# Kernel optimization log

Hardware: AMD Instinct MI355X
Metric: run time of the kernel (lower is better)

The kernel has to match this reference:

```python
import jax, jax.numpy as jnp
import numpy as np

D_MODEL = 512
EPS = 1e-5  # torch LayerNorm default


def _layernorm(x, g, b):
    mu = jnp.mean(x, axis=-1, keepdims=True)
    var = jnp.mean(jnp.square(x - mu), axis=-1, keepdims=True)
    return (x - mu) * jax.lax.rsqrt(var + EPS) * g + b


def setup_inputs() -> dict:
    key = jax.random.key(0)
    ks = jax.random.split(key, 12)
    d = D_MODEL
    s = 1.0 / np.sqrt(d)
    s4 = 1.0 / np.sqrt(4 * d)
    return {
        "x": jax.random.normal(ks[0], (4, 4096, d), dtype=jnp.float32),
        "Wq": jax.random.uniform(ks[1], (d, d), jnp.float32, -s, s),
        "bq": jax.random.uniform(ks[2], (d,), jnp.float32, -s, s),
        "Wk": jax.random.uniform(ks[3], (d, d), jnp.float32, -s, s),
        "bk": jax.random.uniform(ks[4], (d,), jnp.float32, -s, s),
        "Wv": jax.random.uniform(ks[5], (d, d), jnp.float32, -s, s),
        "bv": jax.random.uniform(ks[6], (d,), jnp.float32, -s, s),
        "g1": jnp.ones((d,), jnp.float32),
        "b1": jnp.zeros((d,), jnp.float32),
        "g2": jnp.ones((d,), jnp.float32),
        "b2": jnp.zeros((d,), jnp.float32),
        "W1": jax.random.uniform(ks[7], (d, 4 * d), jnp.float32, -s, s),
        "bf1": jax.random.uniform(ks[8], (4 * d,), jnp.float32, -s, s),
        "W2": jax.random.uniform(ks[9], (4 * d, d), jnp.float32, -s4, s4),
        "bf2": jax.random.uniform(ks[10], (d,), jnp.float32, -s4, s4),
    }


def reference(x, Wq, bq, Wk, bk, Wv, bv, g1, b1, g2, b2, W1, bf1, W2, bf2):
    # QKV projections: [b, s, d]
    Q = jnp.einsum("bsd,de->bse", x, Wq) + bq
    K = jnp.einsum("bsd,de->bse", x, Wk) + bk
    V = jnp.einsum("bsd,de->bse", x, Wv) + bv
    scale = 1.0 / jnp.sqrt(jnp.float32(K.shape[-1]))
    scores = jnp.einsum("bqd,bkd->bqk", Q, K) * scale  # [b, s, s]
    attn = jax.nn.softmax(scores, axis=-1)
    att = jnp.einsum("bqk,bkd->bqd", attn, V)
    x = _layernorm(x + att, g1, b1)
    h = jax.nn.relu(jnp.einsum("bsd,df->bsf", x, W1) + bf1)
    ffn = jnp.einsum("bsf,fd->bsd", h, W2) + bf2
    return _layernorm(x + ffn, g2, b2)
```

## Files before the change

### kernel.cpp

```cpp
#include <hip/hip_runtime.h>
#include <hip/hip_bf16.h>

typedef unsigned short u16;
typedef short bf16x8 __attribute__((ext_vector_type(8)));
typedef float f32x4 __attribute__((ext_vector_type(4)));

__device__ __forceinline__ float b2f(u16 u) {
  union { float f; unsigned int i; } v; v.i = ((unsigned int)u) << 16; return v.f;
}
__device__ __forceinline__ u16 f2b(float f) {
  union { float f; unsigned int i; } v; v.f = f;
  unsigned int r = v.i + 0x7fffu + ((v.i >> 16) & 1u);
  return (u16)(r >> 16);
}
__device__ __forceinline__ u16 to_b(float v) { return f2b(v); }
__device__ __forceinline__ u16 to_b(u16 v) { return v; }
__device__ __forceinline__ float to_f(float v) { return v; }
__device__ __forceinline__ float to_f(u16 v) { return b2f(v); }

__device__ __forceinline__ void gl_lds16(const u16* g, u16* l) {
  __builtin_amdgcn_global_load_lds(
      (const __attribute__((address_space(1))) unsigned int*)g,
      (__attribute__((address_space(3))) unsigned int*)l, 16, 0, 0);
}

template <bool RELU, bool ATOMIC>
__global__ __launch_bounds__(256)
void gemm_nt(const u16* __restrict__ A, const u16* __restrict__ Bt,
             const float* __restrict__ bias, void* __restrict__ Cv,
             int N, int K, int nsplit, int lda, int ldb, int ldc,
             long sA, long sB, long sC, float scale) {
  __shared__ __align__(16) u16 As[128 * 64];
  __shared__ __align__(16) u16 Bs[128 * 64];
  const int z = blockIdx.z;
  const int batch = z / nsplit, split = z - batch * nsplit;
  const int Ks = K / nsplit;
  const u16* Ab = A + (long)batch * sA + (long)split * Ks;
  const u16* Bb = Bt + (long)batch * sB + (long)split * Ks;
  const int m0 = blockIdx.y * 128, n0 = blockIdx.x * 128;
  const int t = threadIdx.x, w = t >> 6, lane = t & 63;
  const int wm = (w >> 1) * 64, wn = (w & 1) * 64;
  const int lr = lane & 15, q = lane >> 4;

  int srow[4], scol[4];
#pragma unroll
  for (int i = 0; i < 4; i++) {
    int n = w * 256 + i * 64 + lane;
    srow[i] = n >> 3;
    scol[i] = (((n & 7) ^ ((n >> 3) & 7)) * 8);
  }

  f32x4 acc[4][4];
#pragma unroll
  for (int i = 0; i < 4; i++)
#pragma unroll
    for (int j = 0; j < 4; j++) acc[i][j] = (f32x4){0.f, 0.f, 0.f, 0.f};

  for (int k0 = 0; k0 < Ks; k0 += 64) {
#pragma unroll
    for (int i = 0; i < 4; i++)
      gl_lds16(Ab + (long)(m0 + srow[i]) * lda + k0 + scol[i], &As[(w * 256 + i * 64) * 8]);
#pragma unroll
    for (int i = 0; i < 4; i++)
      gl_lds16(Bb + (long)(n0 + srow[i]) * ldb + k0 + scol[i], &Bs[(w * 256 + i * 64) * 8]);
    __syncthreads();
#pragma unroll
    for (int kk = 0; kk < 2; kk++) {
      bf16x8 af[4], bfr[4];
#pragma unroll
      for (int i = 0; i < 4; i++) {
        int row = wm + i * 16 + lr;
        af[i] = *(const bf16x8*)&As[row * 64 + (((kk * 4 + q) ^ (row & 7)) * 8)];
      }
#pragma unroll
      for (int j = 0; j < 4; j++) {
        int row = wn + j * 16 + lr;
        bfr[j] = *(const bf16x8*)&Bs[row * 64 + (((kk * 4 + q) ^ (row & 7)) * 8)];
      }
#pragma unroll
      for (int i = 0; i < 4; i++)
#pragma unroll
        for (int j = 0; j < 4; j++)
          acc[i][j] = __builtin_amdgcn_mfma_f32_16x16x32_bf16(af[i], bfr[j], acc[i][j], 0, 0, 0);
    }
    __syncthreads();
  }

#pragma unroll
  for (int j = 0; j < 4; j++) {
    int cg = n0 + wn + j * 16 + lr;
    float bb = (!ATOMIC && bias) ? bias[cg] : 0.0f;
#pragma unroll
    for (int i = 0; i < 4; i++) {
      int rbase = m0 + wm + i * 16 + q * 4;
#pragma unroll
      for (int r = 0; r < 4; r++) {
        float vv = acc[i][j][r] * scale;
        if (ATOMIC) {
          atomicAdd((float*)Cv + (long)batch * sC + (long)(rbase + r) * ldc + cg, vv);
        } else {
          vv += bb;
          if (RELU) vv = fmaxf(vv, 0.0f);
          ((u16*)Cv)[(long)batch * sC + (long)(rbase + r) * ldc + cg] = f2b(vv);
        }
      }
    }
  }
}

__global__ __launch_bounds__(256, 2)
void flash_attn(const u16* __restrict__ QKV, const u16* __restrict__ Vt,
                u16* __restrict__ attp, float* __restrict__ lbp, float scl) {
  __shared__ __align__(16) u16 buf[128 * 128];
  const int qt = blockIdx.x;
  const int half = blockIdx.y;
  const int batch = blockIdx.z;
  const int t = threadIdx.x, w = t >> 6, lane = t & 63;
  const int lr = lane & 15, q = lane >> 4;
  const long rowbase = (long)batch * 4096 + qt * 64;
  const u16* Qrow  = QKV + (rowbase + w * 16 + lr) * 1536;
  const u16* Kbase = QKV + ((long)batch * 4096 + half * 2048) * 1536 + 512;
  const u16* Vtb   = Vt + (long)batch * 512 * 4096 + half * 2048;
  u16* Pw = buf + w * (16 * 136);

  f32x4 O[32];
#pragma unroll
  for (int i = 0; i < 32; i++) O[i] = (f32x4){0.f, 0.f, 0.f, 0.f};
  float lsum[4] = {0.f, 0.f, 0.f, 0.f};

  for (int kv = 0; kv < 16; kv++) {
    f32x4 S[8];
#pragma unroll
    for (int j = 0; j < 8; j++) S[j] = (f32x4){0.f, 0.f, 0.f, 0.f};

    for (int kc = 0; kc < 4; kc++) {
#pragma unroll
      for (int rr = 0; rr < 8; rr++) {
        int n = rr * 256 + t;
        int row = n >> 4, c = (n & 15) ^ (row & 15);
        gl_lds16(Kbase + (long)(kv * 128 + row) * 1536 + kc * 128 + c * 8,
                 &buf[(rr * 256 + w * 64) * 8]);
      }
      bf16x8 Qf[4];
#pragma unroll
      for (int ss = 0; ss < 4; ss++)
        Qf[ss] = *(const bf16x8*)(Qrow + kc * 128 + ss * 32 + q * 8);
      __syncthreads();
#pragma unroll
      for (int ss = 0; ss < 4; ss++)
#pragma unroll
        for (int j = 0; j < 8; j++) {
          int row = j * 16 + lr;
          bf16x8 Kf = *(const bf16x8*)&buf[row * 128 + (((ss * 4 + q) ^ lr) * 8)];
          S[j] = __builtin_amdgcn_mfma_f32_16x16x32_bf16(Qf[ss], Kf, S[j], 0, 0, 0);
        }
      __syncthreads();
    }

    float psum[4] = {0.f, 0.f, 0.f, 0.f};
#pragma unroll
    for (int j = 0; j < 8; j++)
#pragma unroll
      for (int r = 0; r < 4; r++) {
        float e = __expf(S[j][r] * scl);
        psum[r] += e;
        Pw[(q * 4 + r) * 136 + j * 16 + lr] = f2b(e);
      }
#pragma unroll
    for (int r = 0; r < 4; r++) {
#pragma unroll
      for (int o = 1; o < 16; o <<= 1) psum[r] += __shfl_xor(psum[r], o);
      lsum[r] += psum[r];
    }
    bf16x8 Pf[4];
#pragma unroll
    for (int t4 = 0; t4 < 4; t4++)
      Pf[t4] = *(const bf16x8*)&Pw[lr * 136 + t4 * 32 + q * 8];
    __syncthreads();

    for (int dc = 0; dc < 4; dc++) {
#pragma unroll
      for (int rr = 0; rr < 8; rr++) {
        int n = rr * 256 + t;
        int row = n >> 4, c = (n & 15) ^ (row & 15);
        gl_lds16(Vtb + (long)(dc * 128 + row) * 4096 + kv * 128 + c * 8,
                 &buf[(rr * 256 + w * 64) * 8]);
      }
      __syncthreads();
#pragma unroll
      for (int t4 = 0; t4 < 4; t4++)
#pragma unroll
        for (int j = 0; j < 8; j++) {
          int row = j * 16 + lr;
          bf16x8 Vf = *(const bf16x8*)&buf[row * 128 + (((t4 * 4 + q) ^ lr) * 8)];
          O[dc * 8 + j] = __builtin_amdgcn_mfma_f32_16x16x32_bf16(Pf[t4], Vf, O[dc * 8 + j], 0, 0, 0);
        }
      __syncthreads();
    }
  }

  u16* op = attp + (long)half * 16384 * 512;
#pragma unroll
  for (int i = 0; i < 32; i++) {
    int col = (i >> 3) * 128 + (i & 7) * 16 + lr;
#pragma unroll
    for (int r = 0; r < 4; r++)
      op[(rowbase + w * 16 + q * 4 + r) * 512 + col] = f2b(O[i][r]);
  }
  if (lr == 0)
#pragma unroll
    for (int r = 0; r < 4; r++)
      lbp[(long)half * 16384 + rowbase + w * 16 + q * 4 + r] = lsum[r];
}

template <typename TS>
__global__ __launch_bounds__(1024)
void transpose_b(const TS* __restrict__ src, u16* __restrict__ dst,
                 int R, int Cc, int src_ld, long sbs, long dbs) {
  __shared__ u16 tile[32][33];
  int r = blockIdx.y * 32 + threadIdx.y;
  int c = blockIdx.x * 32 + threadIdx.x;
  tile[threadIdx.y][threadIdx.x] = to_b(src[(long)blockIdx.z * sbs + (long)r * src_ld + c]);
  __syncthreads();
  int rr = blockIdx.x * 32 + threadIdx.y;
  int cc = blockIdx.y * 32 + threadIdx.x;
  dst[(long)blockIdx.z * dbs + (long)rr * R + cc] = tile[threadIdx.x][threadIdx.y];
}

__global__ __launch_bounds__(256)
void f32_to_bf16(const float* __restrict__ s, u16* __restrict__ d) {
  long i = ((long)blockIdx.x * 256 + threadIdx.x) * 8;
  float4 a0 = *(const float4*)(s + i);
  float4 a1 = *(const float4*)(s + i + 4);
  u16 tmp[8] = {f2b(a0.x), f2b(a0.y), f2b(a0.z), f2b(a0.w),
                f2b(a1.x), f2b(a1.y), f2b(a1.z), f2b(a1.w)};
  *(uint4*)(d + i) = *(uint4*)tmp;
}

__global__ __launch_bounds__(256)
void add_ln_att(const float* __restrict__ X, const u16* __restrict__ attp,
                const float* __restrict__ lbp,
                const float* __restrict__ g, const float* __restrict__ b,
                u16* __restrict__ O) {
  const int row = blockIdx.x * 4 + (threadIdx.x >> 6);
  const int lane = threadIdx.x & 63;
  const size_t base = (size_t)row * 512 + lane * 8;
  const float inv = 1.0f / (lbp[row] + lbp[16384 + row]);
  uint4 p0 = *(const uint4*)(attp + base);
  uint4 p1 = *(const uint4*)(attp + 16384L * 512 + base);
  const u16* s0 = (const u16*)&p0;
  const u16* s1 = (const u16*)&p1;
  float z[8];
  float s1a = 0.f, s2a = 0.f;
#pragma unroll
  for (int i = 0; i < 8; i++) {
    z[i] = X[base + i] + (b2f(s0[i]) + b2f(s1[i])) * inv;
    s1a += z[i]; s2a += z[i] * z[i];
  }
#pragma unroll
  for (int o = 32; o > 0; o >>= 1) { s1a += __shfl_xor(s1a, o); s2a += __shfl_xor(s2a, o); }
  const float mu = s1a * (1.0f / 512.0f);
  const float var = s2a * (1.0f / 512.0f) - mu * mu;
  const float rstd = rsqrtf(var + 1e-5f);
#pragma unroll
  for (int i = 0; i < 8; i++) {
    int c = lane * 8 + i;
    O[base + i] = f2b((z[i] - mu) * rstd * g[c] + b[c]);
  }
}

template <typename TX, typename TR, bool EB, typename TO>
__global__ __launch_bounds__(256)
void add_ln(const TX* __restrict__ X, const TR* __restrict__ Rr,
            const float* __restrict__ eb,
            const float* __restrict__ g, const float* __restrict__ b,
            TO* __restrict__ O) {
  const int row = blockIdx.x * 4 + (threadIdx.x >> 6);
  const int lane = threadIdx.x & 63;
  const size_t base = (size_t)row * 512 + lane * 8;
  float z[8];
  float s1 = 0.f, s2 = 0.f;
#pragma unroll
  for (int i = 0; i < 8; i++) {
    int c = lane * 8 + i;
    z[i] = to_f(X[base + i]) + to_f(Rr[base + i]) + (EB ? eb[c] : 0.0f);
    s1 += z[i]; s2 += z[i] * z[i];
  }
#pragma unroll
  for (int o = 32; o > 0; o >>= 1) { s1 += __shfl_xor(s1, o); s2 += __shfl_xor(s2, o); }
  const float mu = s1 * (1.0f / 512.0f);
  const float var = s2 * (1.0f / 512.0f) - mu * mu;
  const float rstd = rsqrtf(var + 1e-5f);
#pragma unroll
  for (int i = 0; i < 8; i++) {
    int c = lane * 8 + i;
    float vv = (z[i] - mu) * rstd * g[c] + b[c];
    if (sizeof(TO) == 2) ((u16*)O)[base + i] = f2b(vv);
    else ((float*)O)[base + i] = vv;
  }
}

__global__ __launch_bounds__(256)
void concat3(const float* __restrict__ a, const float* __restrict__ b,
             const float* __restrict__ c, float* __restrict__ o) {
  int i = threadIdx.x + blockIdx.x * 256;
  if (i < 512) o[i] = a[i];
  else if (i < 1024) o[i] = b[i - 512];
  else if (i < 1536) o[i] = c[i - 1024];
}

extern "C" void kernel_launch(void* const* d_in, const int* in_sizes, int n_in,
                              void* d_out, int out_size, void* d_ws, size_t ws_size,
                              hipStream_t stream) {
  const float* x   = (const float*)d_in[0];
  const float* Wq  = (const float*)d_in[1];
  const float* bq  = (const float*)d_in[2];
  const float* Wk  = (const float*)d_in[3];
  const float* bk  = (const float*)d_in[4];
  const float* Wv  = (const float*)d_in[5];
  const float* bv  = (const float*)d_in[6];
  const float* g1  = (const float*)d_in[7];
  const float* b1  = (const float*)d_in[8];
  const float* g2  = (const float*)d_in[9];
  const float* b2  = (const float*)d_in[10];
  const float* W1  = (const float*)d_in[11];
  const float* bf1 = (const float*)d_in[12];
  const float* W2  = (const float*)d_in[13];
  const float* bf2 = (const float*)d_in[14];
  float* out = (float*)d_out;

  char* ws = (char*)d_ws;
  const size_t MB = 1048576;
  u16*   QKV   = (u16*)(ws + 0);
  u16*   Vt    = (u16*)(ws + 48 * MB);
  u16*   attp  = (u16*)(ws + 64 * MB);
  u16*   h     = (u16*)(ws + 64 * MB);
  float* lbp   = (float*)(ws + 128 * MB);
  u16*   x1    = (u16*)(ws + 129 * MB);
  float* ffnf  = (float*)(ws + 145 * MB);
  u16*   xb    = (u16*)(ws + 145 * MB);
  u16*   wqkvt = (u16*)(ws + 177 * MB);
  u16*   w1t   = wqkvt + 1536 * 512;
  u16*   w2t   = w1t + 2048 * 512;
  float* bqkv  = (float*)(w2t + 512 * 2048);

  dim3 tb(32, 32);
  f32_to_bf16<<<4096, 256, 0, stream>>>(x, xb);
  transpose_b<float><<<dim3(16, 16, 1), tb, 0, stream>>>(Wq, wqkvt,              512, 512, 512, 0, 0);
  transpose_b<float><<<dim3(16, 16, 1), tb, 0, stream>>>(Wk, wqkvt + 512 * 512,  512, 512, 512, 0, 0);
  transpose_b<float><<<dim3(16, 16, 1), tb, 0, stream>>>(Wv, wqkvt + 1024 * 512, 512, 512, 512, 0, 0);
  transpose_b<float><<<dim3(64, 16, 1), tb, 0, stream>>>(W1, w1t, 512, 2048, 2048, 0, 0);
  transpose_b<float><<<dim3(16, 64, 1), tb, 0, stream>>>(W2, w2t, 2048, 512, 512, 0, 0);
  concat3<<<6, 256, 0, stream>>>(bq, bk, bv, bqkv);

  gemm_nt<false, false><<<dim3(12, 128, 1), 256, 0, stream>>>(
      xb, wqkvt, bqkv, QKV, 1536, 512, 1, 512, 512, 1536, 0, 0, 0, 1.0f);

  transpose_b<u16><<<dim3(16, 128, 4), tb, 0, stream>>>(
      QKV + 1024, Vt, 4096, 512, 1536, 4096L * 1536, 512L * 4096);

  const float scl = 0.044194173824159216f;
  flash_attn<<<dim3(64, 2, 4), 256, 0, stream>>>(QKV, Vt, attp, lbp, scl);

  add_ln_att<<<4096, 256, 0, stream>>>(x, attp, lbp, g1, b1, x1);
  gemm_nt<true, false><<<dim3(16, 128, 1), 256, 0, stream>>>(
      x1, w1t, bf1, h, 2048, 512, 1, 512, 512, 2048, 0, 0, 0, 1.0f);
  hipMemsetAsync(ffnf, 0, 32 * MB, stream);
  gemm_nt<false, true><<<dim3(4, 128, 2), 256, 0, stream>>>(
      h, w2t, nullptr, ffnf, 512, 2048, 2, 2048, 2048, 512, 0, 0, 0, 1.0f);
  add_ln<u16, float, true, float><<<4096, 256, 0, stream>>>(
      x1, ffnf, bf2, g2, b2, out);
}
```

Baseline: 610.0 us.

## Split attention KV four ways and replace atomic FFN2 split-K with bf16 partials

The flash attention kernel now splits the key/value range into four quarters instead of two. That doubles the grid, and the launch bound rises to 4 blocks per CU to improve occupancy; the attention add+LayerNorm kernel sums four partial outputs and four row sums. The second FFN GEMM no longer memsets an fp32 buffer and accumulates with atomics. Instead it writes two bf16 split-K partials that a new fused add+LayerNorm kernel combines with the bias. The higher occupancy target may cause register spills in the attention kernel, and the bf16 partials lose some precision.

```diff
diff --git a/kernel.cpp b/kernel.cpp
--- a/kernel.cpp
+++ b/kernel.cpp
@@ -108,19 +108,19 @@
   }
 }
 
-__global__ __launch_bounds__(256, 2)
+__global__ __launch_bounds__(256, 4)
 void flash_attn(const u16* __restrict__ QKV, const u16* __restrict__ Vt,
                 u16* __restrict__ attp, float* __restrict__ lbp, float scl) {
   __shared__ __align__(16) u16 buf[128 * 128];
   const int qt = blockIdx.x;
-  const int half = blockIdx.y;
+  const int quar = blockIdx.y;
   const int batch = blockIdx.z;
   const int t = threadIdx.x, w = t >> 6, lane = t & 63;
   const int lr = lane & 15, q = lane >> 4;
   const long rowbase = (long)batch * 4096 + qt * 64;
   const u16* Qrow  = QKV + (rowbase + w * 16 + lr) * 1536;
-  const u16* Kbase = QKV + ((long)batch * 4096 + half * 2048) * 1536 + 512;
-  const u16* Vtb   = Vt + (long)batch * 512 * 4096 + half * 2048;
+  const u16* Kbase = QKV + ((long)batch * 4096 + quar * 1024) * 1536 + 512;
+  const u16* Vtb   = Vt + (long)batch * 512 * 4096 + quar * 1024;
   u16* Pw = buf + w * (16 * 136);
 
   f32x4 O[32];
@@ -128,7 +128,7 @@
   for (int i = 0; i < 32; i++) O[i] = (f32x4){0.f, 0.f, 0.f, 0.f};
   float lsum[4] = {0.f, 0.f, 0.f, 0.f};
 
-  for (int kv = 0; kv < 16; kv++) {
+  for (int kv = 0; kv < 8; kv++) {
     f32x4 S[8];
 #pragma unroll
     for (int j = 0; j < 8; j++) S[j] = (f32x4){0.f, 0.f, 0.f, 0.f};
@@ -199,7 +199,7 @@
     }
   }
 
-  u16* op = attp + (long)half * 16384 * 512;
+  u16* op = attp + (long)quar * 16384 * 512;
 #pragma unroll
   for (int i = 0; i < 32; i++) {
     int col = (i >> 3) * 128 + (i & 7) * 16 + lr;
@@ -210,7 +210,7 @@
   if (lr == 0)
 #pragma unroll
     for (int r = 0; r < 4; r++)
-      lbp[(long)half * 16384 + rowbase + w * 16 + q * 4 + r] = lsum[r];
+      lbp[(long)quar * 16384 + rowbase + w * 16 + q * 4 + r] = lsum[r];
 }
 
 template <typename TS>
@@ -245,16 +245,20 @@
   const int row = blockIdx.x * 4 + (threadIdx.x >> 6);
   const int lane = threadIdx.x & 63;
   const size_t base = (size_t)row * 512 + lane * 8;
-  const float inv = 1.0f / (lbp[row] + lbp[16384 + row]);
-  uint4 p0 = *(const uint4*)(attp + base);
-  uint4 p1 = *(const uint4*)(attp + 16384L * 512 + base);
-  const u16* s0 = (const u16*)&p0;
-  const u16* s1 = (const u16*)&p1;
+  const float inv = 1.0f / (lbp[row] + lbp[16384 + row] + lbp[32768 + row] + lbp[49152 + row]);
+  float acc[8] = {0, 0, 0, 0, 0, 0, 0, 0};
+#pragma unroll
+  for (int p = 0; p < 4; p++) {
+    uint4 pv = *(const uint4*)(attp + (long)p * 16384 * 512 + base);
+    const u16* s = (const u16*)&pv;
+#pragma unroll
+    for (int i = 0; i < 8; i++) acc[i] += b2f(s[i]);
+  }
   float z[8];
   float s1a = 0.f, s2a = 0.f;
 #pragma unroll
   for (int i = 0; i < 8; i++) {
-    z[i] = X[base + i] + (b2f(s0[i]) + b2f(s1[i])) * inv;
+    z[i] = X[base + i] + acc[i] * inv;
     s1a += z[i]; s2a += z[i] * z[i];
   }
 #pragma unroll
@@ -269,34 +273,37 @@
   }
 }
 
-template <typename TX, typename TR, bool EB, typename TO>
-__global__ __launch_bounds__(256)
-void add_ln(const TX* __restrict__ X, const TR* __restrict__ Rr,
-            const float* __restrict__ eb,
-            const float* __restrict__ g, const float* __restrict__ b,
-            TO* __restrict__ O) {
+__global__ __launch_bounds__(256)
+void add_ln_ffn(const u16* __restrict__ X, const u16* __restrict__ P0,
+                const u16* __restrict__ P1, const float* __restrict__ eb,
+                const float* __restrict__ g, const float* __restrict__ b,
+                float* __restrict__ O) {
   const int row = blockIdx.x * 4 + (threadIdx.x >> 6);
   const int lane = threadIdx.x & 63;
   const size_t base = (size_t)row * 512 + lane * 8;
+  uint4 xv = *(const uint4*)(X + base);
+  uint4 a0 = *(const uint4*)(P0 + base);
+  uint4 a1 = *(const uint4*)(P1 + base);
+  const u16* xs = (const u16*)&xv;
+  const u16* s0 = (const u16*)&a0;
+  const u16* s1 = (const u16*)&a1;
   float z[8];
-  float s1 = 0.f, s2 = 0.f;
+  float s1a = 0.f, s2a = 0.f;
 #pragma unroll
   for (int i = 0; i < 8; i++) {
     int c = lane * 8 + i;
-    z[i] = to_f(X[base + i]) + to_f(Rr[base + i]) + (EB ? eb[c] : 0.0f);
-    s1 += z[i]; s2 += z[i] * z[i];
-  }
-#pragma unroll
-  for (int o = 32; o > 0; o >>= 1) { s1 += __shfl_xor(s1, o); s2 += __shfl_xor(s2, o); }
-  const float mu = s1 * (1.0f / 512.0f);
-  const float var = s2 * (1.0f / 512.0f) - mu * mu;
+    z[i] = b2f(xs[i]) + b2f(s0[i]) + b2f(s1[i]) + eb[c];
+    s1a += z[i]; s2a += z[i] * z[i];
+  }
+#pragma unroll
+  for (int o = 32; o > 0; o >>= 1) { s1a += __shfl_xor(s1a, o); s2a += __shfl_xor(s2a, o); }
+  const float mu = s1a * (1.0f / 512.0f);
+  const float var = s2a * (1.0f / 512.0f) - mu * mu;
   const float rstd = rsqrtf(var + 1e-5f);
 #pragma unroll
   for (int i = 0; i < 8; i++) {
     int c = lane * 8 + i;
-    float vv = (z[i] - mu) * rstd * g[c] + b[c];
-    if (sizeof(TO) == 2) ((u16*)O)[base + i] = f2b(vv);
-    else ((float*)O)[base + i] = vv;
+    O[base + i] = (z[i] - mu) * rstd * g[c] + b[c];
   }
 }
 
@@ -337,7 +344,7 @@
   u16*   h     = (u16*)(ws + 64 * MB);
   float* lbp   = (float*)(ws + 128 * MB);
   u16*   x1    = (u16*)(ws + 129 * MB);
-  float* ffnf  = (float*)(ws + 145 * MB);
+  u16*   ffnp  = (u16*)(ws + 145 * MB);
   u16*   xb    = (u16*)(ws + 145 * MB);
   u16*   wqkvt = (u16*)(ws + 177 * MB);
   u16*   w1t   = wqkvt + 1536 * 512;
@@ -360,14 +367,14 @@
       QKV + 1024, Vt, 4096, 512, 1536, 4096L * 1536, 512L * 4096);
 
   const float scl = 0.044194173824159216f;
-  flash_attn<<<dim3(64, 2, 4), 256, 0, stream>>>(QKV, Vt, attp, lbp, scl);
+  flash_attn<<<dim3(64, 4, 4), 256, 0, stream>>>(QKV, Vt, attp, lbp, scl);
 
   add_ln_att<<<4096, 256, 0, stream>>>(x, attp, lbp, g1, b1, x1);
   gemm_nt<true, false><<<dim3(16, 128, 1), 256, 0, stream>>>(
       x1, w1t, bf1, h, 2048, 512, 1, 512, 512, 2048, 0, 0, 0, 1.0f);
-  hipMemsetAsync(ffnf, 0, 32 * MB, stream);
-  gemm_nt<false, true><<<dim3(4, 128, 2), 256, 0, stream>>>(
-      h, w2t, nullptr, ffnf, 512, 2048, 2, 2048, 2048, 512, 0, 0, 0, 1.0f);
-  add_ln<u16, float, true, float><<<4096, 256, 0, stream>>>(
-      x1, ffnf, bf2, g2, b2, out);
-}
+  gemm_nt<false, false><<<dim3(4, 128, 2), 256, 0, stream>>>(
+      h, w2t, nullptr, ffnp, 512, 1024, 1, 2048, 2048, 512,
+      1024, 1024, 16384L * 512, 1.0f);
+  add_ln_ffn<<<4096, 256, 0, stream>>>(
+      x1, ffnp, ffnp + 16384L * 512, bf2, g2, b2, out);
+}
```

After: 812.5 us. 33.2% more time.
